# Performance work log

Hardware: AMD Instinct MI355X
Metric: run time of the kernel (lower is better)

Reference implementation:

```python
import jax, jax.numpy as jnp
import numpy as np

ALPHA = 0.25  # synaptic decay
BETA = 1.0    # membrane decay
SURR_SCALE = 100.0  # SuperSpike surrogate sharpness

@jax.custom_vjp
def spike_fn(x):
    # Heaviside forward (hard threshold), surrogate gradient backward
    return (x > 0).astype(x.dtype)

def _spike_fwd(x):
    return spike_fn(x), x

def _spike_bwd(x, g):
    surr = 1.0 / (1.0 + SURR_SCALE * jnp.abs(x)) ** 2
    return (g * surr,)

spike_fn.defvjp(_spike_fwd, _spike_bwd)


def setup_inputs() -> dict:
    key = jax.random.key(0)
    k1, k2, k3 = jax.random.split(key, 3)
    N, L, D, T = 2048, 100, 512, 1024
    X = jax.random.normal(k1, (N, L, D), dtype=jnp.float32)
    W = jax.random.normal(k2, (D, T), dtype=jnp.float32) / np.sqrt(D)
    U = jax.random.normal(k3, (T, T), dtype=jnp.float32) / np.sqrt(T)
    return {"X": X, "W": W, "U": U}


def reference(X, W, U):
    # Faithful port of bdnn2.getH: LIF spiking recurrence with hard reset.
    N, l, d = X.shape
    T = W.shape[1]
    dtype = X.dtype
    # precompute input drive for all timesteps: [N, l, T]
    h1_in = jnp.einsum('nld,dt->nlt', X, W)

    def step(carry, h_t):
        syn, mem, out_prev = carry
        h1 = h_t + out_prev @ U                 # recurrent input
        out = spike_fn(mem - 1.0)               # spike from CURRENT mem (pre-update)
        rst = jax.lax.stop_gradient(out)        # rst = out.detach()
        new_syn = ALPHA * syn + h1
        new_mem = (BETA * mem + syn) * (1.0 - rst)
        return (new_syn, new_mem, out), out

    init = (jnp.zeros((N, T), dtype), jnp.zeros((N, T), dtype), jnp.zeros((N, T), dtype))
    # scan over time axis
    _, spk = jax.lax.scan(step, init, jnp.swapaxes(h1_in, 0, 1))  # spk: [l, N, T]
    H = jnp.sum(spk, axis=0) / l                                  # [N, T]
    return H
```

## Files before the change

kernel.cpp:

```cpp
#include <hip/hip_runtime.h>
#include <math.h>

#define NSAMP  2048
#define LSTEPS 100
#define DDIM   512
#define TDIM   1024
#define SB     8
#define NTHR   512
#define JJ     2

__global__ __launch_bounds__(NTHR)
void snn_fused(const float* __restrict__ X, const float* __restrict__ W,
               const float* __restrict__ U, float* __restrict__ out)
{
#pragma clang fp contract(off)
    __shared__ float xs[SB][DDIM];
    __shared__ unsigned int msk[2][SB][TDIM / 32];
    __shared__ unsigned short klist[2][SB][TDIM];
    __shared__ int kcnt[2][SB][2];

    const int tid  = threadIdx.x;
    const int lane = tid & 63;
    const int wv   = tid >> 6;
    const int n0   = blockIdx.x * SB;

    float syn[JJ][SB], mem[JJ][SB];
    int   cnt[JJ][SB];
#pragma unroll
    for (int q = 0; q < JJ; ++q)
#pragma unroll
        for (int s = 0; s < SB; ++s) { syn[q][s] = 0.0f; mem[q][s] = 0.0f; cnt[q][s] = 0; }

    ((unsigned int*)msk)[tid] = 0u;
    if (tid < 32) ((int*)kcnt)[tid] = 0;

    const float* w0 = W + tid;
    const float* w1 = W + tid + NTHR;
    const float* u0 = U + tid;
    const float* u1 = U + tid + NTHR;

    auto gather2 = [&](const unsigned short* ls, int beg, int end,
                       float& A0, float& A1) {
        float a0 = 0.0f, a1 = 0.0f;
        int i = beg;
        const int n = end - beg;
        if (n >= 4) {
            const int nm = n & ~3;
            int ka = (int)ls[i] << 10,     kb = (int)ls[i + 1] << 10;
            int kc = (int)ls[i + 2] << 10, kd = (int)ls[i + 3] << 10;
            float c0a = u0[ka], c1a = u1[ka];
            float c0b = u0[kb], c1b = u1[kb];
            float c0c = u0[kc], c1c = u1[kc];
            float c0d = u0[kd], c1d = u1[kd];
            for (; i + 4 < beg + nm; i += 4) {
                int ea = (int)ls[i + 4] << 10, eb = (int)ls[i + 5] << 10;
                int ec = (int)ls[i + 6] << 10, ed = (int)ls[i + 7] << 10;
                float d0a = u0[ea], d1a = u1[ea];
                float d0b = u0[eb], d1b = u1[eb];
                float d0c = u0[ec], d1c = u1[ec];
                float d0d = u0[ed], d1d = u1[ed];
                a0 = __fadd_rn(a0, c0a); a1 = __fadd_rn(a1, c1a);
                a0 = __fadd_rn(a0, c0b); a1 = __fadd_rn(a1, c1b);
                a0 = __fadd_rn(a0, c0c); a1 = __fadd_rn(a1, c1c);
                a0 = __fadd_rn(a0, c0d); a1 = __fadd_rn(a1, c1d);
                c0a = d0a; c1a = d1a; c0b = d0b; c1b = d1b;
                c0c = d0c; c1c = d1c; c0d = d0d; c1d = d1d;
            }
            a0 = __fadd_rn(a0, c0a); a1 = __fadd_rn(a1, c1a);
            a0 = __fadd_rn(a0, c0b); a1 = __fadd_rn(a1, c1b);
            a0 = __fadd_rn(a0, c0c); a1 = __fadd_rn(a1, c1c);
            a0 = __fadd_rn(a0, c0d); a1 = __fadd_rn(a1, c1d);
            i = beg + nm;
        }
        for (; i < end; ++i) {
            const int k = (int)ls[i] << 10;
            a0 = __fadd_rn(a0, u0[k]);
            a1 = __fadd_rn(a1, u1[k]);
        }
        A0 = a0; A1 = a1;
    };

    int p = 0;
    for (int t = 0; t < LSTEPS; ++t) {
#pragma unroll
        for (int c = 0; c < 2; ++c) {
            const int cc = tid + c * NTHR;
            const int s  = cc >> 7;
            const int k4 = (cc & 127) << 2;
            *(float4*)&xs[s][k4] =
                *(const float4*)(X + ((size_t)(n0 + s) * LSTEPS + t) * DDIM + k4);
        }
        __syncthreads();

        float a32[JJ][SB];
#pragma unroll
        for (int q = 0; q < JJ; ++q)
#pragma unroll
            for (int s = 0; s < SB; ++s) a32[q][s] = 0.0f;

        for (int k4 = 0; k4 < DDIM; k4 += 4) {
            float4 xv[SB];
#pragma unroll
            for (int s = 0; s < SB; ++s) xv[s] = *(const float4*)&xs[s][k4];
            float wv0[4], wv1[4];
#pragma unroll
            for (int e = 0; e < 4; ++e) {
                wv0[e] = w0[(k4 + e) * TDIM];
                wv1[e] = w1[(k4 + e) * TDIM];
            }
#pragma unroll
            for (int s = 0; s < SB; ++s) {
                a32[0][s] = __fadd_rn(a32[0][s], __fmul_rn(wv0[0], xv[s].x));
                a32[0][s] = __fadd_rn(a32[0][s], __fmul_rn(wv0[1], xv[s].y));
                a32[0][s] = __fadd_rn(a32[0][s], __fmul_rn(wv0[2], xv[s].z));
                a32[0][s] = __fadd_rn(a32[0][s], __fmul_rn(wv0[3], xv[s].w));
                a32[1][s] = __fadd_rn(a32[1][s], __fmul_rn(wv1[0], xv[s].x));
                a32[1][s] = __fadd_rn(a32[1][s], __fmul_rn(wv1[1], xv[s].y));
                a32[1][s] = __fadd_rn(a32[1][s], __fmul_rn(wv1[2], xv[s].z));
                a32[1][s] = __fadd_rn(a32[1][s], __fmul_rn(wv1[3], xv[s].w));
            }
        }

        float ua[JJ][SB];
#pragma unroll 1
        for (int s = 0; s < SB; ++s) {
            const unsigned short* ls = klist[p][s];
            const int clo = kcnt[p][s][0];
            const int ct  = kcnt[p][s][1];
            float q00, q01, q10, q11;
            gather2(ls, 0, clo, q00, q01);
            gather2(ls, clo, ct, q10, q11);
            ua[0][s] = __fadd_rn(q00, q10);
            ua[1][s] = __fadd_rn(q01, q11);
        }

        unsigned int ob0 = 0u, ob1 = 0u;
#pragma unroll
        for (int q = 0; q < JJ; ++q)
#pragma unroll
            for (int s = 0; s < SB; ++s) {
                const float h1 = __fadd_rn(a32[q][s], ua[q][s]);
                const bool  o  = (__fadd_rn(mem[q][s], -1.0f) > 0.0f);
                const float sn = __fadd_rn(__fmul_rn(0.25f, syn[q][s]), h1);
                const float mn = o ? 0.0f : __fadd_rn(mem[q][s], syn[q][s]);
                if (o) {
                    cnt[q][s]++;
                    if (q == 0) ob0 |= (1u << s); else ob1 |= (1u << s);
                }
                syn[q][s] = sn;
                mem[q][s] = mn;
            }

        if (tid < SB * (TDIM / 32)) ((unsigned int*)(msk[p ^ 1]))[tid] = 0u;
        __syncthreads();
#pragma unroll
        for (int s = 0; s < SB; ++s) {
            if (ob0 & (1u << s)) atomicOr(&msk[p ^ 1][s][tid >> 5], 1u << (tid & 31));
            if (ob1 & (1u << s)) atomicOr(&msk[p ^ 1][s][16 + (tid >> 5)], 1u << (tid & 31));
        }
        __syncthreads();

        {
            const int pn = p ^ 1;
            const int s  = wv;
            const unsigned wrd = msk[pn][s][lane >> 1];
            const unsigned w16 = (wrd >> ((lane & 1) * 16)) & 0xFFFFu;
            const int c = __popc(w16);
            int x = c;
#pragma unroll
            for (int d = 1; d < 64; d <<= 1) {
                int y = __shfl_up(x, d);
                if (lane >= d) x += y;
            }
            int pre = x - c;
            unsigned bits = w16;
            const int base = lane * 16;
            while (bits) {
                const int b = __ffs(bits) - 1;
                bits &= bits - 1u;
                klist[pn][s][pre++] = (unsigned short)(base + b);
            }
            const int clo = __shfl(x, 31);
            const int ctt = __shfl(x, 63);
            if (lane == 0) { kcnt[pn][s][0] = clo; kcnt[pn][s][1] = ctt; }
        }
        p ^= 1;
    }

#pragma unroll
    for (int q = 0; q < JJ; ++q)
#pragma unroll
        for (int s = 0; s < SB; ++s)
            out[(size_t)(n0 + s) * TDIM + tid + q * NTHR] =
                __fdiv_rn((float)cnt[q][s], 100.0f);
}

extern "C" void kernel_launch(void* const* d_in, const int* in_sizes, int n_in,
                              void* d_out, int out_size, void* d_ws, size_t ws_size,
                              hipStream_t stream) {
    (void)in_sizes; (void)n_in; (void)out_size; (void)d_ws; (void)ws_size;
    const float* X = (const float*)d_in[0];
    const float* W = (const float*)d_in[1];
    const float* U = (const float*)d_in[2];
    float* outp = (float*)d_out;

    dim3 grid(NSAMP / SB);
    dim3 block(NTHR);
    hipLaunchKernelGGL(snn_fused, grid, block, 0, stream, X, W, U, outp);
}
```

Measured before the change: 7.766 ms.

## Use 1024 threads per block with one output column per thread

The block grows from 512 to 1024 threads, so each thread now owns one of the T columns instead of two, which halves per-thread register state and work. The gather loop over spiking indices is widened to 8 loads in flight per batch to keep more memory requests outstanding. Only the first 8 waves build the spike lists. The trade-off is lower per-thread instruction-level parallelism in the dense X·W accumulation and larger blocks, which could limit how many blocks fit per CU.

```diff
diff --git a/kernel.cpp b/kernel.cpp
--- a/kernel.cpp
+++ b/kernel.cpp
@@ -6,8 +6,7 @@
 #define DDIM   512
 #define TDIM   1024
 #define SB     8
-#define NTHR   512
-#define JJ     2
+#define NTHR   1024
 
 __global__ __launch_bounds__(NTHR)
 void snn_fused(const float* __restrict__ X, const float* __restrict__ W,
@@ -24,143 +23,105 @@
     const int wv   = tid >> 6;
     const int n0   = blockIdx.x * SB;
 
-    float syn[JJ][SB], mem[JJ][SB];
-    int   cnt[JJ][SB];
+    float syn[SB], mem[SB];
+    int   cnt[SB];
 #pragma unroll
-    for (int q = 0; q < JJ; ++q)
-#pragma unroll
-        for (int s = 0; s < SB; ++s) { syn[q][s] = 0.0f; mem[q][s] = 0.0f; cnt[q][s] = 0; }
+    for (int s = 0; s < SB; ++s) { syn[s] = 0.0f; mem[s] = 0.0f; cnt[s] = 0; }
 
-    ((unsigned int*)msk)[tid] = 0u;
-    if (tid < 32) ((int*)kcnt)[tid] = 0;
+    if (tid < 512) ((unsigned int*)msk)[tid] = 0u;
+    if (tid < 32)  ((int*)kcnt)[tid] = 0;
 
-    const float* w0 = W + tid;
-    const float* w1 = W + tid + NTHR;
-    const float* u0 = U + tid;
-    const float* u1 = U + tid + NTHR;
+    const float* wp = W + tid;
+    const float* uC = U + tid;
 
-    auto gather2 = [&](const unsigned short* ls, int beg, int end,
-                       float& A0, float& A1) {
-        float a0 = 0.0f, a1 = 0.0f;
+    auto gather1 = [&](const unsigned short* ls, int beg, int end) -> float {
+        float a = 0.0f;
         int i = beg;
         const int n = end - beg;
-        if (n >= 4) {
-            const int nm = n & ~3;
-            int ka = (int)ls[i] << 10,     kb = (int)ls[i + 1] << 10;
-            int kc = (int)ls[i + 2] << 10, kd = (int)ls[i + 3] << 10;
-            float c0a = u0[ka], c1a = u1[ka];
-            float c0b = u0[kb], c1b = u1[kb];
-            float c0c = u0[kc], c1c = u1[kc];
-            float c0d = u0[kd], c1d = u1[kd];
-            for (; i + 4 < beg + nm; i += 4) {
-                int ea = (int)ls[i + 4] << 10, eb = (int)ls[i + 5] << 10;
-                int ec = (int)ls[i + 6] << 10, ed = (int)ls[i + 7] << 10;
-                float d0a = u0[ea], d1a = u1[ea];
-                float d0b = u0[eb], d1b = u1[eb];
-                float d0c = u0[ec], d1c = u1[ec];
-                float d0d = u0[ed], d1d = u1[ed];
-                a0 = __fadd_rn(a0, c0a); a1 = __fadd_rn(a1, c1a);
-                a0 = __fadd_rn(a0, c0b); a1 = __fadd_rn(a1, c1b);
-                a0 = __fadd_rn(a0, c0c); a1 = __fadd_rn(a1, c1c);
-                a0 = __fadd_rn(a0, c0d); a1 = __fadd_rn(a1, c1d);
-                c0a = d0a; c1a = d1a; c0b = d0b; c1b = d1b;
-                c0c = d0c; c1c = d1c; c0d = d0d; c1d = d1d;
+        if (n >= 8) {
+            const int nm = n & ~7;
+            float c[8];
+#pragma unroll
+            for (int j = 0; j < 8; ++j) c[j] = uC[(int)ls[beg + j] << 10];
+            for (i = beg; i + 8 < beg + nm; i += 8) {
+                float d[8];
+#pragma unroll
+                for (int j = 0; j < 8; ++j) d[j] = uC[(int)ls[i + 8 + j] << 10];
+#pragma unroll
+                for (int j = 0; j < 8; ++j) a = __fadd_rn(a, c[j]);
+#pragma unroll
+                for (int j = 0; j < 8; ++j) c[j] = d[j];
             }
-            a0 = __fadd_rn(a0, c0a); a1 = __fadd_rn(a1, c1a);
-            a0 = __fadd_rn(a0, c0b); a1 = __fadd_rn(a1, c1b);
-            a0 = __fadd_rn(a0, c0c); a1 = __fadd_rn(a1, c1c);
-            a0 = __fadd_rn(a0, c0d); a1 = __fadd_rn(a1, c1d);
+#pragma unroll
+            for (int j = 0; j < 8; ++j) a = __fadd_rn(a, c[j]);
             i = beg + nm;
         }
-        for (; i < end; ++i) {
-            const int k = (int)ls[i] << 10;
-            a0 = __fadd_rn(a0, u0[k]);
-            a1 = __fadd_rn(a1, u1[k]);
-        }
-        A0 = a0; A1 = a1;
+        for (; i < end; ++i) a = __fadd_rn(a, uC[(int)ls[i] << 10]);
+        return a;
     };
 
     int p = 0;
     for (int t = 0; t < LSTEPS; ++t) {
-#pragma unroll
-        for (int c = 0; c < 2; ++c) {
-            const int cc = tid + c * NTHR;
-            const int s  = cc >> 7;
-            const int k4 = (cc & 127) << 2;
+        {
+            const int s  = tid >> 7;
+            const int k4 = (tid & 127) << 2;
             *(float4*)&xs[s][k4] =
                 *(const float4*)(X + ((size_t)(n0 + s) * LSTEPS + t) * DDIM + k4);
         }
         __syncthreads();
 
-        float a32[JJ][SB];
+        float a32[SB];
 #pragma unroll
-        for (int q = 0; q < JJ; ++q)
-#pragma unroll
-            for (int s = 0; s < SB; ++s) a32[q][s] = 0.0f;
+        for (int s = 0; s < SB; ++s) a32[s] = 0.0f;
 
         for (int k4 = 0; k4 < DDIM; k4 += 4) {
             float4 xv[SB];
 #pragma unroll
             for (int s = 0; s < SB; ++s) xv[s] = *(const float4*)&xs[s][k4];
-            float wv0[4], wv1[4];
+            float wv0[4];
 #pragma unroll
-            for (int e = 0; e < 4; ++e) {
-                wv0[e] = w0[(k4 + e) * TDIM];
-                wv1[e] = w1[(k4 + e) * TDIM];
-            }
+            for (int e = 0; e < 4; ++e) wv0[e] = wp[(k4 + e) * TDIM];
 #pragma unroll
             for (int s = 0; s < SB; ++s) {
-                a32[0][s] = __fadd_rn(a32[0][s], __fmul_rn(wv0[0], xv[s].x));
-                a32[0][s] = __fadd_rn(a32[0][s], __fmul_rn(wv0[1], xv[s].y));
-                a32[0][s] = __fadd_rn(a32[0][s], __fmul_rn(wv0[2], xv[s].z));
-                a32[0][s] = __fadd_rn(a32[0][s], __fmul_rn(wv0[3], xv[s].w));
-                a32[1][s] = __fadd_rn(a32[1][s], __fmul_rn(wv1[0], xv[s].x));
-                a32[1][s] = __fadd_rn(a32[1][s], __fmul_rn(wv1[1], xv[s].y));
-                a32[1][s] = __fadd_rn(a32[1][s], __fmul_rn(wv1[2], xv[s].z));
-                a32[1][s] = __fadd_rn(a32[1][s], __fmul_rn(wv1[3], xv[s].w));
+                a32[s] = __fadd_rn(a32[s], __fmul_rn(wv0[0], xv[s].x));
+                a32[s] = __fadd_rn(a32[s], __fmul_rn(wv0[1], xv[s].y));
+                a32[s] = __fadd_rn(a32[s], __fmul_rn(wv0[2], xv[s].z));
+                a32[s] = __fadd_rn(a32[s], __fmul_rn(wv0[3], xv[s].w));
             }
         }
 
-        float ua[JJ][SB];
+        float ua[SB];
 #pragma unroll 1
         for (int s = 0; s < SB; ++s) {
             const unsigned short* ls = klist[p][s];
             const int clo = kcnt[p][s][0];
             const int ct  = kcnt[p][s][1];
-            float q00, q01, q10, q11;
-            gather2(ls, 0, clo, q00, q01);
-            gather2(ls, clo, ct, q10, q11);
-            ua[0][s] = __fadd_rn(q00, q10);
-            ua[1][s] = __fadd_rn(q01, q11);
+            const float P0 = gather1(ls, 0, clo);
+            const float P1 = gather1(ls, clo, ct);
+            ua[s] = __fadd_rn(P0, P1);
         }
 
-        unsigned int ob0 = 0u, ob1 = 0u;
+        unsigned int ob = 0u;
 #pragma unroll
-        for (int q = 0; q < JJ; ++q)
-#pragma unroll
-            for (int s = 0; s < SB; ++s) {
-                const float h1 = __fadd_rn(a32[q][s], ua[q][s]);
-                const bool  o  = (__fadd_rn(mem[q][s], -1.0f) > 0.0f);
-                const float sn = __fadd_rn(__fmul_rn(0.25f, syn[q][s]), h1);
-                const float mn = o ? 0.0f : __fadd_rn(mem[q][s], syn[q][s]);
-                if (o) {
-                    cnt[q][s]++;
-                    if (q == 0) ob0 |= (1u << s); else ob1 |= (1u << s);
-                }
-                syn[q][s] = sn;
-                mem[q][s] = mn;
-            }
+        for (int s = 0; s < SB; ++s) {
+            const float h1 = __fadd_rn(a32[s], ua[s]);
+            const bool  o  = (__fadd_rn(mem[s], -1.0f) > 0.0f);
+            const float sn = __fadd_rn(__fmul_rn(0.25f, syn[s]), h1);
+            const float mn = o ? 0.0f : __fadd_rn(mem[s], syn[s]);
+            if (o) { cnt[s]++; ob |= (1u << s); }
+            syn[s] = sn;
+            mem[s] = mn;
+        }
 
         if (tid < SB * (TDIM / 32)) ((unsigned int*)(msk[p ^ 1]))[tid] = 0u;
         __syncthreads();
 #pragma unroll
-        for (int s = 0; s < SB; ++s) {
-            if (ob0 & (1u << s)) atomicOr(&msk[p ^ 1][s][tid >> 5], 1u << (tid & 31));
-            if (ob1 & (1u << s)) atomicOr(&msk[p ^ 1][s][16 + (tid >> 5)], 1u << (tid & 31));
-        }
+        for (int s = 0; s < SB; ++s)
+            if (ob & (1u << s))
+                atomicOr(&msk[p ^ 1][s][tid >> 5], 1u << (tid & 31));
         __syncthreads();
 
-        {
+        if (wv < SB) {
             const int pn = p ^ 1;
             const int s  = wv;
             const unsigned wrd = msk[pn][s][lane >> 1];
@@ -188,11 +149,8 @@
     }
 
 #pragma unroll
-    for (int q = 0; q < JJ; ++q)
-#pragma unroll
-        for (int s = 0; s < SB; ++s)
-            out[(size_t)(n0 + s) * TDIM + tid + q * NTHR] =
-                __fdiv_rn((float)cnt[q][s], 100.0f);
+    for (int s = 0; s < SB; ++s)
+        out[(size_t)(n0 + s) * TDIM + tid] = __fdiv_rn((float)cnt[s], 100.0f);
 }
 
 extern "C" void kernel_launch(void* const* d_in, const int* in_sizes, int n_in,
```

Result: no change. 7.859 ms (+1.2%).
